# Kernel optimization log

Hardware: AMD Instinct MI355X
Metric: run time of the kernel (lower is better)

The kernel has to match this reference:

```python
import jax, jax.numpy as jnp
import numpy as np

B, C, H, W = 32, 17, 256, 256


def setup_inputs() -> dict:
    key = jax.random.key(0)
    k1, k2 = jax.random.split(key)
    inp = jax.random.normal(k1, (B, C, H, W), dtype=jnp.float32)
    tgt = jax.random.normal(k2, (B, C, H, W), dtype=jnp.float32)
    masks = jnp.zeros((B, C, H, W), dtype=bool)  # unused by forward
    hull = jnp.zeros((B, 1, H, W), dtype=bool)   # unused by forward
    return {"input": inp, "target": tgt, "masks": masks, "hull": hull}


def reference(input, target, masks, hull):
    # m1: per-(batch, channel) mask of positive target pixels
    m1 = target > 0.0                                  # [B,C,H,W] bool
    # m2: per-batch OR over channels, broadcast back to every channel.
    # (replaces the original O(B*C) Python double loop)
    m2 = jnp.any(m1, axis=1, keepdims=True)            # [B,1,H,W] bool
    diff = jnp.abs(input - target)                     # [B,C,H,W]
    f32 = jnp.float32
    # masked means without data-dependent shapes: sum(mask*diff)/sum(mask)
    mean1 = jnp.sum(jnp.where(m1, diff, f32(0))) / jnp.sum(m1).astype(f32)
    cnt2 = jnp.sum(m2).astype(f32) * f32(diff.shape[1])  # broadcast over C channels
    mean2 = jnp.sum(jnp.where(m2, diff, f32(0))) / cnt2
    return (mean1 + mean2) / f32(2)
```

## Files before the change

### kernel.cpp

```cpp
#include <hip/hip_runtime.h>


#define QPB      16384
#define N_CH     17
#define N_BATCH  32
#define N_QUADS  (N_BATCH * QPB)
#define N_BLOCKS 2048
#define PF       3

struct Slot {
    float s1;
    float s2;
    unsigned int c1;
    unsigned int c2;
};

__global__ __launch_bounds__(256, 8) void heatloss_stage1(
    const float* __restrict__ inp, const float* __restrict__ tgt,
    Slot* __restrict__ slots) {

    const int blk = (blockIdx.x & 7) * (N_BLOCKS / 8) + (blockIdx.x >> 3);
    const int q = blk * 256 + threadIdx.x;
    const int b = q >> 14;
    const int r = q & (QPB - 1);

    const float4* __restrict__ tp = (const float4*)tgt + (size_t)b * (N_CH * QPB) + r;
    const float4* __restrict__ xp = (const float4*)inp + (size_t)b * (N_CH * QPB) + r;

    float4 tb[PF], xb[PF];
    #pragma unroll
    for (int i = 0; i < PF; ++i) {
        tb[i] = tp[(size_t)i * QPB];
        xb[i] = xp[(size_t)i * QPB];
    }

    float s1 = 0.0f;
    unsigned int c1 = 0u;
    float sa0 = 0.f, sa1 = 0.f, sa2 = 0.f, sa3 = 0.f;
    bool a0 = false, a1 = false, a2 = false, a3 = false;

    #pragma unroll
    for (int c = 0; c < N_CH; ++c) {
        const int slot = c % PF;
        float4 t = tb[slot];
        float4 x = xb[slot];
        if (c + PF < N_CH) {
            tb[slot] = tp[(size_t)(c + PF) * QPB];
            xb[slot] = xp[(size_t)(c + PF) * QPB];
        }
        float d0 = fabsf(x.x - t.x);
        float d1 = fabsf(x.y - t.y);
        float d2 = fabsf(x.z - t.z);
        float d3 = fabsf(x.w - t.w);
        bool p0 = t.x > 0.f, p1 = t.y > 0.f, p2 = t.z > 0.f, p3 = t.w > 0.f;
        sa0 += d0; sa1 += d1; sa2 += d2; sa3 += d3;
        s1 += p0 ? d0 : 0.f;  c1 += p0 ? 1u : 0u;  a0 = a0 || p0;
        s1 += p1 ? d1 : 0.f;  c1 += p1 ? 1u : 0u;  a1 = a1 || p1;
        s1 += p2 ? d2 : 0.f;  c1 += p2 ? 1u : 0u;  a2 = a2 || p2;
        s1 += p3 ? d3 : 0.f;  c1 += p3 ? 1u : 0u;  a3 = a3 || p3;
    }
    float s2 = (a0 ? sa0 : 0.f) + (a1 ? sa1 : 0.f) + (a2 ? sa2 : 0.f) + (a3 ? sa3 : 0.f);
    unsigned int c2 = (a0 ? 1u : 0u) + (a1 ? 1u : 0u) + (a2 ? 1u : 0u) + (a3 ? 1u : 0u);

    #pragma unroll
    for (int off = 32; off > 0; off >>= 1) {
        s1 += __shfl_down(s1, off);
        s2 += __shfl_down(s2, off);
        c1 += __shfl_down(c1, off);
        c2 += __shfl_down(c2, off);
    }

    __shared__ float ls1[4], ls2[4];
    __shared__ unsigned int lc1[4], lc2[4];
    const int wave = threadIdx.x >> 6;
    const int lane = threadIdx.x & 63;
    if (lane == 0) {
        ls1[wave] = s1; ls2[wave] = s2;
        lc1[wave] = c1; lc2[wave] = c2;
    }
    __syncthreads();
    if (threadIdx.x == 0) {
        Slot sl;
        sl.s1 = ls1[0] + ls1[1] + ls1[2] + ls1[3];
        sl.s2 = ls2[0] + ls2[1] + ls2[2] + ls2[3];
        sl.c1 = lc1[0] + lc1[1] + lc1[2] + lc1[3];
        sl.c2 = lc2[0] + lc2[1] + lc2[2] + lc2[3];
        slots[blockIdx.x] = sl;
    }
}

__global__ __launch_bounds__(256) void heatloss_stage2(
    const Slot* __restrict__ slots, float* __restrict__ out) {

    float s1 = 0.f, s2 = 0.f;
    unsigned int c1 = 0u, c2 = 0u;
    for (int i = threadIdx.x; i < N_BLOCKS; i += 256) {
        Slot sl = slots[i];
        s1 += sl.s1; s2 += sl.s2; c1 += sl.c1; c2 += sl.c2;
    }
    #pragma unroll
    for (int off = 32; off > 0; off >>= 1) {
        s1 += __shfl_down(s1, off);
        s2 += __shfl_down(s2, off);
        c1 += __shfl_down(c1, off);
        c2 += __shfl_down(c2, off);
    }
    __shared__ float ls1[4], ls2[4];
    __shared__ unsigned int lc1[4], lc2[4];
    const int wave = threadIdx.x >> 6;
    const int lane = threadIdx.x & 63;
    if (lane == 0) {
        ls1[wave] = s1; ls2[wave] = s2;
        lc1[wave] = c1; lc2[wave] = c2;
    }
    __syncthreads();
    if (threadIdx.x == 0) {
        float S1 = ls1[0] + ls1[1] + ls1[2] + ls1[3];
        float S2 = ls2[0] + ls2[1] + ls2[2] + ls2[3];
        float C1 = (float)(lc1[0] + lc1[1] + lc1[2] + lc1[3]);
        float C2 = (float)(lc2[0] + lc2[1] + lc2[2] + lc2[3]);
        float mean1 = S1 / C1;
        float mean2 = S2 / (C2 * (float)N_CH);
        out[0] = 0.5f * (mean1 + mean2);
    }
}

extern "C" void kernel_launch(void* const* d_in, const int* in_sizes, int n_in,
                              void* d_out, int out_size, void* d_ws, size_t ws_size,
                              hipStream_t stream) {
    const float* inp = (const float*)d_in[0];
    const float* tgt = (const float*)d_in[1];
    float* out = (float*)d_out;
    Slot* slots = (Slot*)d_ws;

    heatloss_stage1<<<N_BLOCKS, 256, 0, stream>>>(inp, tgt, slots);
    heatloss_stage2<<<1, 256, 0, stream>>>(slots, out);
}
```

Before: 346.9 us.

## Split into mask-build pass with ballot bitmask and flat-streaming main pass

Replaces the per-thread channel-strided loop with a two-pass scheme. The first pass reads the target, packs the per-batch channel-OR positivity into a bitmask using wave ballots and atomicOr, and the second pass streams input and target contiguously, applying that mask. The goal is fully contiguous grid-strided access instead of 17 strided plane reads per thread. The cost is reading the target twice, plus extra kernel launches and atomics.

Measured after the change: 350.9 us. Within noise of the previous version (+1.2%).

```diff
diff --git a/kernel.cpp b/kernel.cpp
--- a/kernel.cpp
+++ b/kernel.cpp
@@ -1,66 +1,91 @@
 #include <hip/hip_runtime.h>
 
 
-#define QPB      16384
-#define N_CH     17
-#define N_BATCH  32
-#define N_QUADS  (N_BATCH * QPB)
-#define N_BLOCKS 2048
-#define PF       3
+typedef unsigned long long u64;
+typedef unsigned int u32;
 
-struct Slot {
-    float s1;
-    float s2;
-    unsigned int c1;
-    unsigned int c2;
-};
+#define N_CH       17
+#define QPP        16384
+#define N_PLANES   (32 * N_CH)
+#define N_QUADS    (N_PLANES * QPP)
+#define GRID1      2048
+#define ITERS      17
+#define MASK_WORDS 32768
+#define SLOT_OFF   (MASK_WORDS * 8)
 
-__global__ __launch_bounds__(256, 8) void heatloss_stage1(
-    const float* __restrict__ inp, const float* __restrict__ tgt,
-    Slot* __restrict__ slots) {
+struct Slot { float s1, s2; u32 c1, c2; };
 
-    const int blk = (blockIdx.x & 7) * (N_BLOCKS / 8) + (blockIdx.x >> 3);
-    const int q = blk * 256 + threadIdx.x;
-    const int b = q >> 14;
-    const int r = q & (QPB - 1);
 
-    const float4* __restrict__ tp = (const float4*)tgt + (size_t)b * (N_CH * QPB) + r;
-    const float4* __restrict__ xp = (const float4*)inp + (size_t)b * (N_CH * QPB) + r;
+__global__ __launch_bounds__(256) void mask_zero(u64* __restrict__ mask) {
+    mask[blockIdx.x * 256 + threadIdx.x] = 0ULL;
+}
 
-    float4 tb[PF], xb[PF];
-    #pragma unroll
-    for (int i = 0; i < PF; ++i) {
-        tb[i] = tp[(size_t)i * QPB];
-        xb[i] = xp[(size_t)i * QPB];
+__global__ __launch_bounds__(256) void mask_build(const float* __restrict__ tgt,
+                                                  u64* __restrict__ mask) {
+    const float4* __restrict__ t4 = (const float4*)tgt;
+    int f = blockIdx.x * 256 + threadIdx.x;
+    const int lane = threadIdx.x & 63;
+    #pragma unroll 1
+    for (int it = 0; it < ITERS; ++it, f += GRID1 * 256) {
+        float4 t = t4[f];
+        u64 b0 = __ballot(t.x > 0.f);
+        u64 b1 = __ballot(t.y > 0.f);
+        u64 b2 = __ballot(t.z > 0.f);
+        u64 b3 = __ballot(t.w > 0.f);
+        int plane = f >> 14;
+        int b = plane / N_CH;
+        int grp = b * 256 + ((f & (QPP - 1)) >> 6);
+        if (lane < 4) {
+            u64 w = (lane == 0) ? b0 : (lane == 1) ? b1 : (lane == 2) ? b2 : b3;
+            if (w) atomicOr(&mask[(size_t)grp * 4 + lane], w);
+        }
     }
+}
 
-    float s1 = 0.0f;
-    unsigned int c1 = 0u;
-    float sa0 = 0.f, sa1 = 0.f, sa2 = 0.f, sa3 = 0.f;
-    bool a0 = false, a1 = false, a2 = false, a3 = false;
+__global__ __launch_bounds__(256) void heat_main(const float* __restrict__ inp,
+                                                 const float* __restrict__ tgt,
+                                                 const u64* __restrict__ mask,
+                                                 Slot* __restrict__ slots) {
+    const float4* __restrict__ t4 = (const float4*)tgt;
+    const float4* __restrict__ x4 = (const float4*)inp;
 
-    #pragma unroll
-    for (int c = 0; c < N_CH; ++c) {
-        const int slot = c % PF;
-        float4 t = tb[slot];
-        float4 x = xb[slot];
-        if (c + PF < N_CH) {
-            tb[slot] = tp[(size_t)(c + PF) * QPB];
-            xb[slot] = xp[(size_t)(c + PF) * QPB];
-        }
+    float s1 = 0.f, s2 = 0.f;
+    u32 c1 = 0u, c2 = 0u;
+    int f = blockIdx.x * 256 + threadIdx.x;
+    const int lane = threadIdx.x & 63;
+
+    #pragma unroll 1
+    for (int it = 0; it < ITERS; ++it, f += GRID1 * 256) {
+        float4 t = t4[f];
+        float4 x = x4[f];
+
+        int plane = f >> 14;
+        int b = plane / N_CH;
+        int grp = b * 256 + ((f & (QPP - 1)) >> 6);
+        u32 g = __builtin_amdgcn_readfirstlane((u32)grp);
+        const u64* __restrict__ mw = mask + (size_t)g * 4;
+        u64 w0 = mw[0], w1 = mw[1], w2 = mw[2], w3 = mw[3];
+
         float d0 = fabsf(x.x - t.x);
         float d1 = fabsf(x.y - t.y);
         float d2 = fabsf(x.z - t.z);
         float d3 = fabsf(x.w - t.w);
+
         bool p0 = t.x > 0.f, p1 = t.y > 0.f, p2 = t.z > 0.f, p3 = t.w > 0.f;
-        sa0 += d0; sa1 += d1; sa2 += d2; sa3 += d3;
-        s1 += p0 ? d0 : 0.f;  c1 += p0 ? 1u : 0u;  a0 = a0 || p0;
-        s1 += p1 ? d1 : 0.f;  c1 += p1 ? 1u : 0u;  a1 = a1 || p1;
-        s1 += p2 ? d2 : 0.f;  c1 += p2 ? 1u : 0u;  a2 = a2 || p2;
-        s1 += p3 ? d3 : 0.f;  c1 += p3 ? 1u : 0u;  a3 = a3 || p3;
+        s1 += p0 ? d0 : 0.f;  c1 += p0 ? 1u : 0u;
+        s1 += p1 ? d1 : 0.f;  c1 += p1 ? 1u : 0u;
+        s1 += p2 ? d2 : 0.f;  c1 += p2 ? 1u : 0u;
+        s1 += p3 ? d3 : 0.f;  c1 += p3 ? 1u : 0u;
+
+        u32 m0 = (u32)((w0 >> lane) & 1ULL);
+        u32 m1 = (u32)((w1 >> lane) & 1ULL);
+        u32 m2 = (u32)((w2 >> lane) & 1ULL);
+        u32 m3 = (u32)((w3 >> lane) & 1ULL);
+        s2 += m0 ? d0 : 0.f;  c2 += m0;
+        s2 += m1 ? d1 : 0.f;  c2 += m1;
+        s2 += m2 ? d2 : 0.f;  c2 += m2;
+        s2 += m3 ? d3 : 0.f;  c2 += m3;
     }
-    float s2 = (a0 ? sa0 : 0.f) + (a1 ? sa1 : 0.f) + (a2 ? sa2 : 0.f) + (a3 ? sa3 : 0.f);
-    unsigned int c2 = (a0 ? 1u : 0u) + (a1 ? 1u : 0u) + (a2 ? 1u : 0u) + (a3 ? 1u : 0u);
 
     #pragma unroll
     for (int off = 32; off > 0; off >>= 1) {
@@ -69,15 +94,10 @@
         c1 += __shfl_down(c1, off);
         c2 += __shfl_down(c2, off);
     }
-
     __shared__ float ls1[4], ls2[4];
-    __shared__ unsigned int lc1[4], lc2[4];
+    __shared__ u32 lc1[4], lc2[4];
     const int wave = threadIdx.x >> 6;
-    const int lane = threadIdx.x & 63;
-    if (lane == 0) {
-        ls1[wave] = s1; ls2[wave] = s2;
-        lc1[wave] = c1; lc2[wave] = c2;
-    }
+    if (lane == 0) { ls1[wave] = s1; ls2[wave] = s2; lc1[wave] = c1; lc2[wave] = c2; }
     __syncthreads();
     if (threadIdx.x == 0) {
         Slot sl;
@@ -89,12 +109,11 @@
     }
 }
 
-__global__ __launch_bounds__(256) void heatloss_stage2(
-    const Slot* __restrict__ slots, float* __restrict__ out) {
-
+__global__ __launch_bounds__(256) void final_reduce(const Slot* __restrict__ slots,
+                                                    float* __restrict__ out) {
     float s1 = 0.f, s2 = 0.f;
-    unsigned int c1 = 0u, c2 = 0u;
-    for (int i = threadIdx.x; i < N_BLOCKS; i += 256) {
+    u32 c1 = 0u, c2 = 0u;
+    for (int i = threadIdx.x; i < GRID1; i += 256) {
         Slot sl = slots[i];
         s1 += sl.s1; s2 += sl.s2; c1 += sl.c1; c2 += sl.c2;
     }
@@ -106,13 +125,10 @@
         c2 += __shfl_down(c2, off);
     }
     __shared__ float ls1[4], ls2[4];
-    __shared__ unsigned int lc1[4], lc2[4];
+    __shared__ u32 lc1[4], lc2[4];
     const int wave = threadIdx.x >> 6;
     const int lane = threadIdx.x & 63;
-    if (lane == 0) {
-        ls1[wave] = s1; ls2[wave] = s2;
-        lc1[wave] = c1; lc2[wave] = c2;
-    }
+    if (lane == 0) { ls1[wave] = s1; ls2[wave] = s2; lc1[wave] = c1; lc2[wave] = c2; }
     __syncthreads();
     if (threadIdx.x == 0) {
         float S1 = ls1[0] + ls1[1] + ls1[2] + ls1[3];
@@ -120,7 +136,7 @@
         float C1 = (float)(lc1[0] + lc1[1] + lc1[2] + lc1[3]);
         float C2 = (float)(lc2[0] + lc2[1] + lc2[2] + lc2[3]);
         float mean1 = S1 / C1;
-        float mean2 = S2 / (C2 * (float)N_CH);
+        float mean2 = S2 / C2;
         out[0] = 0.5f * (mean1 + mean2);
     }
 }
@@ -131,8 +147,11 @@
     const float* inp = (const float*)d_in[0];
     const float* tgt = (const float*)d_in[1];
     float* out = (float*)d_out;
-    Slot* slots = (Slot*)d_ws;
+    u64* mask = (u64*)d_ws;
+    Slot* slots = (Slot*)((char*)d_ws + SLOT_OFF);
 
-    heatloss_stage1<<<N_BLOCKS, 256, 0, stream>>>(inp, tgt, slots);
-    heatloss_stage2<<<1, 256, 0, stream>>>(slots, out);
+    mask_zero<<<128, 256, 0, stream>>>(mask);
+    mask_build<<<GRID1, 256, 0, stream>>>(tgt, mask);
+    heat_main<<<GRID1, 256, 0, stream>>>(inp, tgt, mask, slots);
+    final_reduce<<<1, 256, 0, stream>>>(slots, out);
 }
```
